# Optimization experiments

Measured on AMD Instinct MI355X. Metric: run time of the kernel, lower is better.

## Reference

```python
import jax, jax.numpy as jnp
import numpy as np

DIM = 256
B = 8
H = 56
W = 56
K = 2
EPS = 1e-5  # torch BatchNorm2d default eps


def _conv1x1(x, w, b):
    # x: [B,C,H,W], w: [O,C], b: [O]
    return jnp.einsum('oc,bchw->bohw', w, x) + b[None, :, None, None]


def _bn(x, g, be, m, v):
    # inference-mode BatchNorm2d with running stats
    s = g / jnp.sqrt(v + EPS)
    return x * s[None, :, None, None] + (be - m * s)[None, :, None, None]


def _grapher(x, w1, b1, g1, be1, m1, v1, wg, bg, gg, beg, mg, vg, w2, b2, g2, be2, m2, v2):
    # fc1: 1x1 conv + BN
    h = _bn(_conv1x1(x, w1, b1), g1, be1, m1, v1)
    Hh, Ww = h.shape[2], h.shape[3]
    # MRConv4d: running max over circular-shift differences
    # torch.cat([x[:,:,-i:,:], x[:,:,:-i,:]], dim=2) == jnp.roll(x, i, axis=2)
    xj = jnp.zeros_like(h)

    def body_h(c, i):
        return jnp.maximum(c, h - jnp.roll(h, i, axis=2)), None

    xj, _ = jax.lax.scan(body_h, xj, jnp.arange(K, Hh, K))

    def body_w(c, i):
        return jnp.maximum(c, h - jnp.roll(h, i, axis=3)), None

    xj, _ = jax.lax.scan(body_w, xj, jnp.arange(K, Ww, K))

    cat = jnp.concatenate([h, xj], axis=1)  # [B, 2*dim, H, W]
    # MRConv4d.nn: Conv2d(2*dim, 2*dim, 1) -> BN(2*dim) -> GELU (exact erf)
    g = jax.nn.gelu(_bn(_conv1x1(cat, wg, bg), gg, beg, mg, vg), approximate=False)
    # fc2: Conv2d(2*dim, dim, 1) + BN(dim), then residual
    return _bn(_conv1x1(g, w2, b2), g2, be2, m2, v2) + x


def setup_inputs() -> dict:
    key = jax.random.key(0)
    ks = jax.random.split(key, 12)
    d, d2 = DIM, 2 * DIM

    def w(k, o, c):
        return jax.random.normal(k, (o, c), jnp.float32) * np.float32(1.0 / np.sqrt(c))

    return {
        'x': jax.random.normal(ks[0], (B, d, H, W), jnp.float32),
        'w1': w(ks[1], d, d), 'b1': jnp.zeros((d,), jnp.float32),
        'g1': jnp.ones((d,), jnp.float32), 'be1': jnp.zeros((d,), jnp.float32),
        'm1': jax.random.normal(ks[2], (d,), jnp.float32) * 0.1,
        'v1': jax.random.uniform(ks[3], (d,), jnp.float32, 0.5, 1.5),
        'wg': w(ks[4], d2, d2), 'bg': jnp.zeros((d2,), jnp.float32),
        'gg': jnp.ones((d2,), jnp.float32), 'beg': jnp.zeros((d2,), jnp.float32),
        'mg': jax.random.normal(ks[5], (d2,), jnp.float32) * 0.1,
        'vg': jax.random.uniform(ks[6], (d2,), jnp.float32, 0.5, 1.5),
        'w2': w(ks[7], d, d2), 'b2': jnp.zeros((d,), jnp.float32),
        'g2': jnp.ones((d,), jnp.float32), 'be2': jnp.zeros((d,), jnp.float32),
        'm2': jax.random.normal(ks[8], (d,), jnp.float32) * 0.1,
        'v2': jax.random.uniform(ks[9], (d,), jnp.float32, 0.5, 1.5),
    }


def reference(x, w1, b1, g1, be1, m1, v1, wg, bg, gg, beg, mg, vg, w2, b2, g2, be2, m2, v2):
    return _grapher(x, w1, b1, g1, be1, m1, v1, wg, bg, gg, beg, mg, vg, w2, b2, g2, be2, m2, v2)
```

## Files before the change

### kernel.cpp

```cpp
#include <hip/hip_runtime.h>
#include <math.h>

#define SPB 3136
#define NB 8
#define MTOT (NB*SPB)
#define EPS 1e-5f

typedef unsigned short u16;
typedef __attribute__((ext_vector_type(8))) short short8;
typedef __attribute__((ext_vector_type(4))) float float4v;

__device__ __forceinline__ float b2f(u16 v){ unsigned u=((unsigned)v)<<16; float f; __builtin_memcpy(&f,&u,4); return f; }
__device__ __forceinline__ u16 f2b(float f){ unsigned u; __builtin_memcpy(&u,&f,4); u += 0x7fffu + ((u>>16)&1u); return (u16)(u>>16); }
__device__ __forceinline__ float gelu_f(float z){
  float t = 1.5957691216f * z * (1.0f + 0.044715f*z*z);
  return __fdividef(z, 1.0f + __expf(-t));
}

__device__ __forceinline__ void gll16(const u16* g, u16* l){
  __builtin_amdgcn_global_load_lds((const __attribute__((address_space(1))) void*)g,
                                   (__attribute__((address_space(3))) void*)l, 16, 0, 0);
}

__global__ void prep_k(const float* __restrict__ x, u16* __restrict__ xt,
                       const float* __restrict__ w1,const float* __restrict__ wg,const float* __restrict__ w2,
                       const float* b1,const float* g1,const float* be1,const float* m1,const float* v1,
                       const float* bg,const float* gg,const float* beg,const float* mg,const float* vg,
                       const float* b2,const float* g2,const float* be2,const float* m2,const float* v2,
                       u16* __restrict__ w1b,u16* __restrict__ wgb,u16* __restrict__ w2b,float* cst){
  __shared__ float t[32][33];
  if (blockIdx.z < 8) {
    int b = blockIdx.z, ct = blockIdx.y, st = blockIdx.x;
    int ts = threadIdx.x, tc = threadIdx.y;
    #pragma unroll
    for (int i=0;i<4;i++){
      int c = tc + i*8;
      t[c][ts] = x[((size_t)(b*256 + ct*32 + c))*SPB + st*32 + ts];
    }
    __syncthreads();
    #pragma unroll
    for (int i=0;i<4;i++){
      int r = tc + i*8;
      xt[((size_t)(b*SPB + st*32 + r))*256 + ct*32 + ts] = f2b(t[ts][r]);
    }
  } else {
    int tid = threadIdx.y*32 + threadIdx.x;
    int w = ((blockIdx.z-8)*8 + blockIdx.y)*98 + blockIdx.x;
    int i = w*256 + tid;
    if (i < 65536)  w1b[i] = f2b(w1[i]);
    if (i < 262144) wgb[i] = f2b(wg[i]);
    if (i < 131072) w2b[i] = f2b(w2[i]);
    if (i < 256) {
      float s = g1[i]*rsqrtf(v1[i]+EPS);
      cst[i] = s; cst[256+i] = b1[i]*s + be1[i] - m1[i]*s;
      float s2 = g2[i]*rsqrtf(v2[i]+EPS);
      cst[1536+i] = s2; cst[1792+i] = b2[i]*s2 + be2[i] - m2[i]*s2;
    }
    if (i < 512) {
      float s = gg[i]*rsqrtf(vg[i]+EPS);
      cst[512+i] = s; cst[1024+i] = bg[i]*s + beg[i] - mg[i]*s;
    }
  }
}

__global__ __launch_bounds__(256) void minmax_k(const u16* __restrict__ cat, float* __restrict__ rmin, float* __restrict__ cmin){
  int id = blockIdx.x*8 + (threadIdx.x>>5);
  int b = id/56, i = id%56;
  int c0 = (threadIdx.x&31)*8;
  int col = blockIdx.y;
  const u16* base; size_t stride;
  if (!col){ base = cat + ((size_t)(b*SPB + i*56))*512 + c0; stride = 512; }
  else     { base = cat + ((size_t)(b*SPB + i))*512 + c0;    stride = (size_t)56*512; }
  float mE[8], mO[8];
  #pragma unroll
  for (int k=0;k<8;k++){ mE[k]=3.4e38f; mO[k]=3.4e38f; }
  for (int j=0;j<56;j+=2){
    short8 e = *(const short8*)(base + (size_t)j*stride);
    short8 o = *(const short8*)(base + (size_t)(j+1)*stride);
    #pragma unroll
    for (int k=0;k<8;k++){
      mE[k] = fminf(mE[k], b2f((u16)e[k]));
      mO[k] = fminf(mO[k], b2f((u16)o[k]));
    }
  }
  float* out = col ? cmin : rmin;
  float* pE = &out[((size_t)(b*2+0)*56 + i)*256 + c0];
  float* pO = &out[((size_t)(b*2+1)*56 + i)*256 + c0];
  *(float4v*)pE     = (float4v){mE[0],mE[1],mE[2],mE[3]};
  *(float4v*)(pE+4) = (float4v){mE[4],mE[5],mE[6],mE[7]};
  *(float4v*)pO     = (float4v){mO[0],mO[1],mO[2],mO[3]};
  *(float4v*)(pO+4) = (float4v){mO[4],mO[5],mO[6],mO[7]};
}

__global__ __launch_bounds__(256) void xj_k(u16* __restrict__ cat, const float* __restrict__ rmin, const float* __restrict__ cmin){
  int b = blockIdx.y;
  int t = threadIdx.x;
  int s = blockIdx.x*8 + (t>>5);
  int c0 = (t&31)*8;
  int y = s/56, x = s%56;
  size_t idx = ((size_t)(b*SPB + s))*512;
  short8 h8 = *(const short8*)&cat[idx + c0];
  const float* cp = &cmin[((size_t)(b*2+(y&1))*56 + x)*256 + c0];
  const float* rp = &rmin[((size_t)(b*2+(x&1))*56 + y)*256 + c0];
  float4v cv0 = *(const float4v*)cp, cv1 = *(const float4v*)(cp+4);
  float4v rv0 = *(const float4v*)rp, rv1 = *(const float4v*)(rp+4);
  short8 o;
  #pragma unroll
  for (int j=0;j<8;j++){
    float cm = (j<4) ? cv0[j] : cv1[j-4];
    float rm = (j<4) ? rv0[j] : rv1[j-4];
    o[j] = (short)f2b(fmaxf(0.0f, b2f((u16)h8[j]) - fminf(cm, rm)));
  }
  *(short8*)&cat[idx + 256 + c0] = o;
}

__device__ __forceinline__ int xcd_remap(int orig, int nwg){
  int q = nwg >> 3, r = nwg & 7, xc = orig & 7, rest = orig >> 3;
  int base = (xc < r) ? xc*(q+1) : r*(q+1) + (xc-r)*q;
  return base + rest;
}

template<int KTOT, int EPI>
__global__ __launch_bounds__(256,2) void gemm_k(
    const u16* __restrict__ Ain, const u16* __restrict__ Wt,
    const float* __restrict__ scale, const float* __restrict__ bias,
    void* __restrict__ outp, const float* __restrict__ resid)
{
  __shared__ __align__(16) u16 smem[36864];
  const int tid = threadIdx.x;
  const int nwg = gridDim.x * gridDim.y;
  const int flat = blockIdx.y * gridDim.x + blockIdx.x;
  const int s_ = xcd_remap(flat, nwg);
  const int m0 = (s_ / gridDim.y) * 256;
  const int o0 = (s_ % gridDim.y) * 128;
  const int lane = tid & 63, wid = tid >> 6;
  const int quad = lane >> 4, l16 = lane & 15;

  float4v acc[4][8];
  #pragma unroll
  for (int i=0;i<4;i++)
    #pragma unroll
    for (int j=0;j<8;j++) acc[i][j] = (float4v){0.f,0.f,0.f,0.f};

  const int row = tid >> 2;
  const int q8s = ((tid & 3) ^ ((tid >> 3) & 3)) * 8;
  const u16* ga0 = Ain + ((size_t)(m0 + row))*KTOT + q8s;
  const u16* gb0 = Wt  + ((size_t)(o0 + row))*KTOT + q8s;
  u16* l8 = smem + tid*8;

  auto STAGE = [&](int kt, int buf){
    u16* b_ = l8 + buf*12288;
    gll16(ga0 + kt,                     b_);
    gll16(ga0 + (size_t) 64*KTOT + kt,  b_ + 2048);
    gll16(ga0 + (size_t)128*KTOT + kt,  b_ + 4096);
    gll16(ga0 + (size_t)192*KTOT + kt,  b_ + 6144);
    gll16(gb0 + kt,                     b_ + 8192);
    gll16(gb0 + (size_t) 64*KTOT + kt,  b_ + 10240);
  };
  const int swz = (l16 >> 1) & 3;
  auto COMPUTE = [&](int buf){
    const u16* A_ = smem + buf*12288;
    const u16* B_ = A_ + 8192;
    const int kq = (quad ^ swz) * 8;
    short8 af[4], bfr[8];
    #pragma unroll
    for (int im=0;im<4;im++) af[im]  = *(const short8*)&A_[(wid*64+im*16+l16)*32 + kq];
    #pragma unroll
    for (int in=0;in<8;in++) bfr[in] = *(const short8*)&B_[(in*16+l16)*32 + kq];
    #pragma unroll
    for (int im=0;im<4;im++)
      #pragma unroll
      for (int in=0;in<8;in++)
        acc[im][in] = __builtin_amdgcn_mfma_f32_16x16x32_bf16(af[im], bfr[in], acc[im][in], 0, 0, 0);
  };

  constexpr int NIT = KTOT / 32;
  STAGE(0, 0);
  STAGE(32, 1);
  #pragma unroll
  for (int t = 0; t < NIT; ++t) {
    __builtin_amdgcn_sched_barrier(0);
    if (t + 1 < NIT) asm volatile("s_waitcnt vmcnt(6) lgkmcnt(0)" ::: "memory");
    else             asm volatile("s_waitcnt vmcnt(0) lgkmcnt(0)" ::: "memory");
    __builtin_amdgcn_s_barrier();
    __builtin_amdgcn_sched_barrier(0);
    if (t + 2 < NIT) STAGE((t+2)*32, (t+2)%3);
    COMPUTE(t%3);
  }
  __syncthreads();

  if (EPI == 1 || EPI == 2) {
    u16* tile = smem;
    #pragma unroll
    for (int im=0;im<4;im++)
      #pragma unroll
      for (int in=0;in<8;in++){
        int ol = in*16 + l16;
        float sc = scale[o0+ol], bi = bias[o0+ol];
        #pragma unroll
        for (int r=0;r<4;r++){
          float v = acc[im][in][r]*sc + bi;
          if (EPI==2) v = gelu_f(v);
          tile[(wid*64+im*16+quad*4+r)*128 + ol] = f2b(v);
        }
      }
    __syncthreads();
    u16* op = (u16*)outp;
    #pragma unroll
    for (int p=0;p<16;p++){
      int chunk = p*256 + tid;
      int rr = chunk >> 4, off = (chunk & 15)*8;
      *(uint4*)&op[((size_t)(m0 + rr))*512 + o0 + off] = *(const uint4*)&tile[rr*128 + off];
    }
  } else {
    float* ftile = (float*)smem;
    float* op = (float*)outp;
    #pragma unroll
    for (int h=0; h<2; h++){
      #pragma unroll
      for (int im=0;im<4;im++)
        #pragma unroll
        for (int in4=0;in4<4;in4++){
          int in = h*4 + in4;
          int c64 = in4*16 + l16;
          int og = o0 + h*64 + c64;
          float sc = scale[og], bi = bias[og];
          float4v v;
          #pragma unroll
          for (int r=0;r<4;r++) v[r] = acc[im][in][r]*sc + bi;
          *(float4v*)&ftile[c64*260 + wid*64 + im*16 + quad*4] = v;
        }
      __syncthreads();
      #pragma unroll
      for (int p=0;p<16;p++){
        int chunk = p*256 + tid;
        int rr = chunk >> 6, off = (chunk & 63)*4;
        int m = m0 + off;
        int b = m / SPB, s = m - b*SPB;
        size_t g = ((size_t)(b*256 + o0 + h*64 + rr))*SPB + s;
        float4v v = *(const float4v*)&ftile[rr*260 + off];
        v.x += resid[g]; v.y += resid[g+1]; v.z += resid[g+2]; v.w += resid[g+3];
        *(float4v*)&op[g] = v;
      }
      __syncthreads();
    }
  }
}

extern "C" void kernel_launch(void* const* d_in, const int* in_sizes, int n_in,
                              void* d_out, int out_size, void* d_ws, size_t ws_size,
                              hipStream_t stream)
{
  const float* x  = (const float*)d_in[0];
  const float* w1 = (const float*)d_in[1];
  const float* b1 = (const float*)d_in[2];
  const float* g1 = (const float*)d_in[3];
  const float* be1= (const float*)d_in[4];
  const float* m1 = (const float*)d_in[5];
  const float* v1 = (const float*)d_in[6];
  const float* wg = (const float*)d_in[7];
  const float* bg = (const float*)d_in[8];
  const float* gg = (const float*)d_in[9];
  const float* beg= (const float*)d_in[10];
  const float* mg = (const float*)d_in[11];
  const float* vg = (const float*)d_in[12];
  const float* w2 = (const float*)d_in[13];
  const float* b2 = (const float*)d_in[14];
  const float* g2 = (const float*)d_in[15];
  const float* be2= (const float*)d_in[16];
  const float* m2 = (const float*)d_in[17];
  const float* v2 = (const float*)d_in[18];

  char* ws = (char*)d_ws;
  size_t off = 0;
  auto alloc = [&](size_t bytes){ void* p = ws + off; off += (bytes + 255) & ~(size_t)255; return p; };
  u16* xt    = (u16*)alloc((size_t)MTOT*256*2);
  u16* catt  = (u16*)alloc((size_t)MTOT*512*2);
  u16* gt    = (u16*)alloc((size_t)MTOT*512*2);
  u16* w1b   = (u16*)alloc((size_t)65536*2);
  u16* wgb   = (u16*)alloc((size_t)262144*2);
  u16* w2b   = (u16*)alloc((size_t)131072*2);
  float* cst = (float*)alloc((size_t)2048*4);
  float* rmin= (float*)alloc((size_t)NB*2*56*256*4);
  float* cmin= (float*)alloc((size_t)NB*2*56*256*4);

  hipLaunchKernelGGL(prep_k, dim3(98,8,10), dim3(32,8), 0, stream,
                     x, xt, w1,wg,w2, b1,g1,be1,m1,v1, bg,gg,beg,mg,vg, b2,g2,be2,m2,v2,
                     w1b,wgb,w2b, cst);
  hipLaunchKernelGGL((gemm_k<256,1>), dim3(98,2), dim3(256), 0, stream,
                     xt, w1b, cst+0, cst+256, (void*)catt, (const float*)nullptr);
  hipLaunchKernelGGL(minmax_k, dim3(56,2), dim3(256), 0, stream, catt, rmin, cmin);
  hipLaunchKernelGGL(xj_k, dim3(392, NB), dim3(256), 0, stream, catt, rmin, cmin);
  hipLaunchKernelGGL((gemm_k<512,2>), dim3(98,4), dim3(256), 0, stream,
                     catt, wgb, cst+512, cst+1024, (void*)gt, (const float*)nullptr);
  hipLaunchKernelGGL((gemm_k<512,3>), dim3(98,2), dim3(256), 0, stream,
                     gt, w2b, cst+1536, cst+1792, d_out, x);
}
```

Before: 185.9 us.

## Pad activation and weight row strides and parallelize min reduction across blocks

Activation and weight buffers get padded leading dimensions (288 and 544 instead of 256 and 512). The goal is to break power-of-two strides that cause channel and bank conflicts in the GEMM global-to-LDS loads. The row/column min kernel is also rewritten to launch one block per (batch,line) instead of eight lines per block. It splits the 56-element scan across 8 thread slices and finishes with a shared-memory reduction, raising parallelism from 112 blocks to 896. The padding adds some memory footprint and requires every kernel that indexes these buffers to use the new strides consistently.

```diff
diff --git a/kernel.cpp b/kernel.cpp
--- a/kernel.cpp
+++ b/kernel.cpp
@@ -5,6 +5,8 @@
 #define NB 8
 #define MTOT (NB*SPB)
 #define EPS 1e-5f
+#define XT_LD  288
+#define CAT_LD 544
 
 typedef unsigned short u16;
 typedef __attribute__((ext_vector_type(8))) short short8;
@@ -41,15 +43,15 @@
     #pragma unroll
     for (int i=0;i<4;i++){
       int r = tc + i*8;
-      xt[((size_t)(b*SPB + st*32 + r))*256 + ct*32 + ts] = f2b(t[ts][r]);
+      xt[((size_t)(b*SPB + st*32 + r))*XT_LD + ct*32 + ts] = f2b(t[ts][r]);
     }
   } else {
     int tid = threadIdx.y*32 + threadIdx.x;
     int w = ((blockIdx.z-8)*8 + blockIdx.y)*98 + blockIdx.x;
     int i = w*256 + tid;
-    if (i < 65536)  w1b[i] = f2b(w1[i]);
-    if (i < 262144) wgb[i] = f2b(wg[i]);
-    if (i < 131072) w2b[i] = f2b(w2[i]);
+    if (i < 65536)  w1b[(i>>8)*XT_LD  + (i&255)] = f2b(w1[i]);
+    if (i < 262144) wgb[(i>>9)*CAT_LD + (i&511)] = f2b(wg[i]);
+    if (i < 131072) w2b[(i>>9)*CAT_LD + (i&511)] = f2b(w2[i]);
     if (i < 256) {
       float s = g1[i]*rsqrtf(v1[i]+EPS);
       cst[i] = s; cst[256+i] = b1[i]*s + be1[i] - m1[i]*s;
@@ -64,32 +66,37 @@
 }
 
 __global__ __launch_bounds__(256) void minmax_k(const u16* __restrict__ cat, float* __restrict__ rmin, float* __restrict__ cmin){
-  int id = blockIdx.x*8 + (threadIdx.x>>5);
-  int b = id/56, i = id%56;
-  int c0 = (threadIdx.x&31)*8;
+  __shared__ float red[8][256];
+  int b = blockIdx.x/56, i = blockIdx.x%56;
   int col = blockIdx.y;
+  int slice = threadIdx.x >> 5;
+  int c0 = (threadIdx.x & 31) * 8;
   const u16* base; size_t stride;
-  if (!col){ base = cat + ((size_t)(b*SPB + i*56))*512 + c0; stride = 512; }
-  else     { base = cat + ((size_t)(b*SPB + i))*512 + c0;    stride = (size_t)56*512; }
-  float mE[8], mO[8];
-  #pragma unroll
-  for (int k=0;k<8;k++){ mE[k]=3.4e38f; mO[k]=3.4e38f; }
-  for (int j=0;j<56;j+=2){
-    short8 e = *(const short8*)(base + (size_t)j*stride);
-    short8 o = *(const short8*)(base + (size_t)(j+1)*stride);
-    #pragma unroll
-    for (int k=0;k<8;k++){
-      mE[k] = fminf(mE[k], b2f((u16)e[k]));
-      mO[k] = fminf(mO[k], b2f((u16)o[k]));
-    }
-  }
-  float* out = col ? cmin : rmin;
-  float* pE = &out[((size_t)(b*2+0)*56 + i)*256 + c0];
-  float* pO = &out[((size_t)(b*2+1)*56 + i)*256 + c0];
-  *(float4v*)pE     = (float4v){mE[0],mE[1],mE[2],mE[3]};
-  *(float4v*)(pE+4) = (float4v){mE[4],mE[5],mE[6],mE[7]};
-  *(float4v*)pO     = (float4v){mO[0],mO[1],mO[2],mO[3]};
-  *(float4v*)(pO+4) = (float4v){mO[4],mO[5],mO[6],mO[7]};
+  if (!col){ base = cat + ((size_t)(b*SPB + i*56))*CAT_LD + c0; stride = CAT_LD; }
+  else     { base = cat + ((size_t)(b*SPB + i))*CAT_LD + c0;    stride = (size_t)56*CAT_LD; }
+  float m[8];
+  #pragma unroll
+  for (int k=0;k<8;k++) m[k]=3.4e38f;
+  #pragma unroll
+  for (int jj=0;jj<7;jj++){
+    short8 v = *(const short8*)(base + (size_t)(slice + jj*8)*stride);
+    #pragma unroll
+    for (int k=0;k<8;k++) m[k] = fminf(m[k], b2f((u16)v[k]));
+  }
+  #pragma unroll
+  for (int k=0;k<8;k++) red[slice][c0+k] = m[k];
+  __syncthreads();
+  int t = threadIdx.x;
+  if (t < 64){
+    int par = t >> 5;
+    int cc = (t & 31) * 8;
+    float* out = col ? cmin : rmin;
+    float* p = &out[((size_t)(b*2+par)*56 + i)*256 + cc];
+    #pragma unroll
+    for (int k=0;k<8;k++)
+      p[k] = fminf(fminf(red[par][cc+k], red[par+2][cc+k]),
+                   fminf(red[par+4][cc+k], red[par+6][cc+k]));
+  }
 }
 
 __global__ __launch_bounds__(256) void xj_k(u16* __restrict__ cat, const float* __restrict__ rmin, const float* __restrict__ cmin){
@@ -98,7 +105,7 @@
   int s = blockIdx.x*8 + (t>>5);
   int c0 = (t&31)*8;
   int y = s/56, x = s%56;
-  size_t idx = ((size_t)(b*SPB + s))*512;
+  size_t idx = ((size_t)(b*SPB + s))*CAT_LD;
   short8 h8 = *(const short8*)&cat[idx + c0];
   const float* cp = &cmin[((size_t)(b*2+(y&1))*56 + x)*256 + c0];
   const float* rp = &rmin[((size_t)(b*2+(x&1))*56 + y)*256 + c0];
@@ -120,7 +127,7 @@
   return base + rest;
 }
 
-template<int KTOT, int EPI>
+template<int KTOT, int LDA, int LDB, int EPI>
 __global__ __launch_bounds__(256,2) void gemm_k(
     const u16* __restrict__ Ain, const u16* __restrict__ Wt,
     const float* __restrict__ scale, const float* __restrict__ bias,
@@ -144,18 +151,18 @@
 
   const int row = tid >> 2;
   const int q8s = ((tid & 3) ^ ((tid >> 3) & 3)) * 8;
-  const u16* ga0 = Ain + ((size_t)(m0 + row))*KTOT + q8s;
-  const u16* gb0 = Wt  + ((size_t)(o0 + row))*KTOT + q8s;
+  const u16* ga0 = Ain + ((size_t)(m0 + row))*LDA + q8s;
+  const u16* gb0 = Wt  + ((size_t)(o0 + row))*LDB + q8s;
   u16* l8 = smem + tid*8;
 
   auto STAGE = [&](int kt, int buf){
     u16* b_ = l8 + buf*12288;
     gll16(ga0 + kt,                     b_);
-    gll16(ga0 + (size_t) 64*KTOT + kt,  b_ + 2048);
-    gll16(ga0 + (size_t)128*KTOT + kt,  b_ + 4096);
-    gll16(ga0 + (size_t)192*KTOT + kt,  b_ + 6144);
+    gll16(ga0 + (size_t) 64*LDA + kt,   b_ + 2048);
+    gll16(ga0 + (size_t)128*LDA + kt,   b_ + 4096);
+    gll16(ga0 + (size_t)192*LDA + kt,   b_ + 6144);
     gll16(gb0 + kt,                     b_ + 8192);
-    gll16(gb0 + (size_t) 64*KTOT + kt,  b_ + 10240);
+    gll16(gb0 + (size_t) 64*LDB + kt,   b_ + 10240);
   };
   const int swz = (l16 >> 1) & 3;
   auto COMPUTE = [&](int buf){
@@ -210,7 +217,7 @@
     for (int p=0;p<16;p++){
       int chunk = p*256 + tid;
       int rr = chunk >> 4, off = (chunk & 15)*8;
-      *(uint4*)&op[((size_t)(m0 + rr))*512 + o0 + off] = *(const uint4*)&tile[rr*128 + off];
+      *(uint4*)&op[((size_t)(m0 + rr))*CAT_LD + o0 + off] = *(const uint4*)&tile[rr*128 + off];
     }
   } else {
     float* ftile = (float*)smem;
@@ -274,12 +281,12 @@
   char* ws = (char*)d_ws;
   size_t off = 0;
   auto alloc = [&](size_t bytes){ void* p = ws + off; off += (bytes + 255) & ~(size_t)255; return p; };
-  u16* xt    = (u16*)alloc((size_t)MTOT*256*2);
-  u16* catt  = (u16*)alloc((size_t)MTOT*512*2);
-  u16* gt    = (u16*)alloc((size_t)MTOT*512*2);
-  u16* w1b   = (u16*)alloc((size_t)65536*2);
-  u16* wgb   = (u16*)alloc((size_t)262144*2);
-  u16* w2b   = (u16*)alloc((size_t)131072*2);
+  u16* xt    = (u16*)alloc((size_t)MTOT*XT_LD*2);
+  u16* catt  = (u16*)alloc((size_t)MTOT*CAT_LD*2);
+  u16* gt    = (u16*)alloc((size_t)MTOT*CAT_LD*2);
+  u16* w1b   = (u16*)alloc((size_t)256*XT_LD*2);
+  u16* wgb   = (u16*)alloc((size_t)512*CAT_LD*2);
+  u16* w2b   = (u16*)alloc((size_t)256*CAT_LD*2);
   float* cst = (float*)alloc((size_t)2048*4);
   float* rmin= (float*)alloc((size_t)NB*2*56*256*4);
   float* cmin= (float*)alloc((size_t)NB*2*56*256*4);
@@ -287,12 +294,12 @@
   hipLaunchKernelGGL(prep_k, dim3(98,8,10), dim3(32,8), 0, stream,
                      x, xt, w1,wg,w2, b1,g1,be1,m1,v1, bg,gg,beg,mg,vg, b2,g2,be2,m2,v2,
                      w1b,wgb,w2b, cst);
-  hipLaunchKernelGGL((gemm_k<256,1>), dim3(98,2), dim3(256), 0, stream,
+  hipLaunchKernelGGL((gemm_k<256,XT_LD,XT_LD,1>), dim3(98,2), dim3(256), 0, stream,
                      xt, w1b, cst+0, cst+256, (void*)catt, (const float*)nullptr);
-  hipLaunchKernelGGL(minmax_k, dim3(56,2), dim3(256), 0, stream, catt, rmin, cmin);
+  hipLaunchKernelGGL(minmax_k, dim3(NB*56,2), dim3(256), 0, stream, catt, rmin, cmin);
   hipLaunchKernelGGL(xj_k, dim3(392, NB), dim3(256), 0, stream, catt, rmin, cmin);
-  hipLaunchKernelGGL((gemm_k<512,2>), dim3(98,4), dim3(256), 0, stream,
+  hipLaunchKernelGGL((gemm_k<512,CAT_LD,CAT_LD,2>), dim3(98,4), dim3(256), 0, stream,
                      catt, wgb, cst+512, cst+1024, (void*)gt, (const float*)nullptr);
-  hipLaunchKernelGGL((gemm_k<512,3>), dim3(98,2), dim3(256), 0, stream,
+  hipLaunchKernelGGL((gemm_k<512,CAT_LD,CAT_LD,3>), dim3(98,2), dim3(256), 0, stream,
                      gt, w2b, cst+1536, cst+1792, d_out, x);
 }
```

New measurement: 179.4 us. 1.04x faster.
